# Optimization experiments

Measured on AMD Instinct MI355X. Metric: run time of the kernel, lower is better.

## Reference

```python
import jax, jax.numpy as jnp
import numpy as np
from jax import lax

B = 64          # graphs per batch
N0 = 1024       # nodes per graph (equal-sized graphs -> static topk shapes)
DEG = 16        # avg degree
E = B * N0 * DEG
D_IN, D_H, D_OUT = 100, 128, 256
RATIO, EPS = 0.5, 1e-5


def _seg_sum(v, idx, n):
    return jax.ops.segment_sum(v, idx, num_segments=n)


def _gcn(x, src, dst, w_e, W, b, n):
    h = x @ W
    deg = 1.0 + _seg_sum(w_e, dst, n)          # +1 for self-loop
    dinv = lax.rsqrt(deg)
    norm = (dinv[src] * dinv[dst] * w_e)[:, None]
    return _seg_sum(h[src] * norm, dst, n) + h / deg[:, None] + b


def _graphnorm(x, w, bias, ms, nb, k):
    # PyG GraphNorm: per-graph mean/var with learnable mean_scale
    xg = x.reshape(nb, k, -1)
    mean = xg.mean(1, keepdims=True)
    sub = xg - ms * mean
    var = (sub * sub).mean(1, keepdims=True)
    return (w * sub * lax.rsqrt(var + EPS) + bias).reshape(nb * k, -1)


def _topk(x, src, dst, emask, p, nb, n_per):
    # TopKPooling (min_score=None): score = tanh(x.p/||p||), keep top ceil(r*n)
    k = int(np.ceil(RATIO * n_per))
    score = jnp.tanh((x @ p) / jnp.linalg.norm(p))
    vals, idx = lax.top_k(score.reshape(nb, n_per), k)            # [nb, k]
    perm = (idx + (jnp.arange(nb) * n_per)[:, None]).reshape(-1)
    x_new = x[perm] * vals.reshape(-1)[:, None]
    mapping = jnp.full((nb * n_per,), -1, jnp.int32).at[perm].set(
        jnp.arange(nb * k, dtype=jnp.int32))
    ns, nd = mapping[src], mapping[dst]
    valid = emask & (ns >= 0) & (nd >= 0)   # filter_adj as a persistent mask
    return x_new, jnp.where(valid, ns, 0), jnp.where(valid, nd, 0), valid, k


def _forward(x, edge_index, W1, b1, W2, b2, W3, b3,
             gn1_w, gn1_b, gn1_ms, gn2_w, gn2_b, gn2_ms,
             gn3_w, gn3_b, gn3_ms, p1, p2, p3):
    src, dst = edge_index[0], edge_index[1]
    emask = jnp.ones(src.shape, bool)
    Ws, bs = (W1, W2, W3), (b1, b2, b3)
    gw = (gn1_w, gn2_w, gn3_w)
    gb = (gn1_b, gn2_b, gn3_b)
    gm = (gn1_ms, gn2_ms, gn3_ms)
    ps = (p1, p2, p3)
    n_per = N0
    for i in range(3):
        n = B * n_per
        x = _gcn(x, src, dst, emask.astype(x.dtype), Ws[i], bs[i], n)
        x = _graphnorm(x, gw[i], gb[i], gm[i], B, n_per)
        x = jax.nn.relu(x)              # dropout: identity in eval mode
        x, src, dst, emask, n_per = _topk(x, src, dst, emask, ps[i], B, n_per)
    xg = x.reshape(B, n_per, D_OUT)
    # global mean/max pool then concat -> [B, 2*D_OUT]
    return jnp.concatenate([xg.mean(1), xg.max(1)], axis=1)


def setup_inputs():
    key = jax.random.key(0)
    ks = jax.random.split(key, 20)
    x = jax.random.normal(ks[0], (B * N0, D_IN), jnp.float32)
    # random edges within each graph, then offset by graph base index
    e = jax.random.randint(ks[1], (2, B, N0 * DEG), 0, N0, jnp.int32)
    edge_index = (e + (jnp.arange(B, dtype=jnp.int32) * N0)[None, :, None]).reshape(2, -1)
    batch = jnp.repeat(jnp.arange(B, dtype=jnp.int32), N0)
    inp = dict(x=x, edge_index=edge_index, batch=batch)
    dims = [(D_IN, D_H), (D_H, D_H), (D_H, D_OUT)]
    for i, (di, do) in enumerate(dims, 1):
        inp[f"W{i}"] = jax.random.normal(ks[1 + i], (di, do), jnp.float32) / np.sqrt(di)
        inp[f"b{i}"] = jnp.zeros((do,), jnp.float32)
        inp[f"gn{i}_w"] = jnp.ones((do,), jnp.float32)
        inp[f"gn{i}_b"] = jnp.zeros((do,), jnp.float32)
        inp[f"gn{i}_ms"] = jnp.ones((do,), jnp.float32)
        inp[f"p{i}"] = jax.random.normal(ks[10 + i], (do,), jnp.float32)
    return inp


def reference(x, edge_index, batch, W1, b1, W2, b2, W3, b3,
              gn1_w, gn1_b, gn1_ms, gn2_w, gn2_b, gn2_ms,
              gn3_w, gn3_b, gn3_ms, p1, p2, p3):
    del batch  # equal-sized graphs: grouping is encoded by constants B, N0
    return _forward(x, edge_index, W1, b1, W2, b2, W3, b3,
                    gn1_w, gn1_b, gn1_ms, gn2_w, gn2_b, gn2_ms,
                    gn3_w, gn3_b, gn3_ms, p1, p2, p3)
```

## Files before the change

kernel.cpp:

```cpp
#include <hip/hip_runtime.h>

#define GN_EPS 1e-5f

constexpr int NB   = 64;
constexpr int EPG  = 16384;
constexpr int ETOT = NB * EPG;
constexpr int NTOT = 64 * 1024;

__global__ void cmap_init_kernel(int* __restrict__ cmap) {
    int i = blockIdx.x * blockDim.x + threadIdx.x;
    if (i < NTOT) cmap[i] = i;
}

template <int NPG>
__global__ __launch_bounds__(1024) void csr_build_kernel(
        const int* __restrict__ ei, int* __restrict__ cmap,
        const int* __restrict__ mapping, int do_compose,
        int* __restrict__ cnt, int* __restrict__ offs, float* __restrict__ dinv,
        int2* __restrict__ csr_pack) {
    __shared__ int   lcnt[NPG];
    __shared__ float sdv[NPG];
    __shared__ int   wsum[16];
    constexpr int NW = NPG / 64;
    const int g = blockIdx.x;
    const int t = threadIdx.x;
    const int ebase = g * EPG;
    constexpr int EPT = EPG / 1024;

    if (do_compose) {
        int i = g * 1024 + t;
        int c = cmap[i];
        cmap[i] = (c >= 0) ? mapping[c] : -1;
    }
    for (int i = t; i < NPG; i += 1024) lcnt[i] = 0;
    __syncthreads();

    int ms_[EPT], md_[EPT];
#pragma unroll
    for (int i = 0; i < EPT; i++) {
        int e = ebase + t + i * 1024;
        int s = cmap[ei[e]];
        int d = cmap[ei[ETOT + e]];
        bool ok = (s >= 0) && (d >= 0);
        ms_[i] = ok ? s : -1;
        md_[i] = ok ? (d - g * NPG) : 0;
        if (ok) atomicAdd(&lcnt[d - g * NPG], 1);
    }
    __syncthreads();

    const int lane = t & 63;
    const int wid  = t >> 6;
    int orig = (t < NPG) ? lcnt[t] : 0;
    int v = orig;
#pragma unroll
    for (int d = 1; d < 64; d <<= 1) {
        int u = __shfl_up(v, d);
        if (lane >= d) v += u;
    }
    if (lane == 63) wsum[wid] = v;
    __syncthreads();
    if (wid == 0) {
        int wv = (lane < NW) ? wsum[lane] : 0;
#pragma unroll
        for (int d = 1; d < 16; d <<= 1) {
            int u = __shfl_up(wv, d);
            if (lane >= d) wv += u;
        }
        if (lane < NW) wsum[lane] = wv;
    }
    __syncthreads();
    if (t < NPG) {
        int incl = v + ((wid > 0) ? wsum[wid - 1] : 0);
        int excl = incl - orig;
        float dv = rsqrtf(1.0f + (float)orig);
        cnt[g * NPG + t]  = orig;
        offs[g * NPG + t] = ebase + excl;
        dinv[g * NPG + t] = dv;
        sdv[t] = dv;
        lcnt[t] = excl;
    }
    __syncthreads();

#pragma unroll
    for (int i = 0; i < EPT; i++) {
        int s = ms_[i];
        if (s >= 0) {
            int pos = atomicAdd(&lcnt[md_[i]], 1);
            csr_pack[ebase + pos] = make_int2(s, __float_as_int(sdv[s - g * 1024 >= 0 && NPG == 1024 ? s - g * NPG : s - g * NPG]));
        }
    }
}

template <int D4>
__global__ __launch_bounds__(256) void gather_kernel(
        const float* __restrict__ x, const int* __restrict__ cnt,
        const int* __restrict__ offs, const float* __restrict__ dinv,
        const int2* __restrict__ csr_pack, float* __restrict__ z, int n, int bpg) {
    constexpr int GRP = 8;
    constexpr int NPB = 256 / GRP;
    constexpr int CPL = 4;
    int bid   = blockIdx.x;
    int xcd   = bid & 7;
    int slot  = bid >> 3;
    int graph = xcd + 8 * (slot / bpg);
    int local = slot % bpg;
    int vb    = graph * bpg + local;

    int grp  = threadIdx.x / GRP;
    int lane = threadIdx.x % GRP;
    int v = vb * NPB + grp;
    if (v >= n) return;

    const float4* x4 = reinterpret_cast<const float4*>(x);
    int st = offs[v];
    int c  = cnt[v];
    float dv = dinv[v];

    int f4_[CPL];
    bool act[CPL];
#pragma unroll
    for (int i = 0; i < CPL; i++) {
        f4_[i] = lane + GRP * i;
        act[i] = f4_[i] < D4;
    }

    float4 acc[CPL];
#pragma unroll
    for (int i = 0; i < CPL; i++) {
        if (act[i]) {
            float4 xv = x4[(size_t)v * D4 + f4_[i]];
            acc[i] = {xv.x * dv, xv.y * dv, xv.z * dv, xv.w * dv};
        } else {
            acc[i] = {0.f, 0.f, 0.f, 0.f};
        }
    }

    int j = 0;
    for (; j + 2 <= c; j += 2) {
        int2 p0 = csr_pack[st + j];
        int2 p1 = csr_pack[st + j + 1];
        float d0 = __int_as_float(p0.y);
        float d1 = __int_as_float(p1.y);
        size_t r0 = (size_t)p0.x * D4;
        size_t r1 = (size_t)p1.x * D4;
#pragma unroll
        for (int i = 0; i < CPL; i++) {
            if (!act[i]) continue;
            float4 h0 = x4[r0 + f4_[i]];
            float4 h1 = x4[r1 + f4_[i]];
            acc[i].x += h0.x * d0 + h1.x * d1;
            acc[i].y += h0.y * d0 + h1.y * d1;
            acc[i].z += h0.z * d0 + h1.z * d1;
            acc[i].w += h0.w * d0 + h1.w * d1;
        }
    }
    if (j < c) {
        int2 p0 = csr_pack[st + j];
        float d0 = __int_as_float(p0.y);
        size_t r0 = (size_t)p0.x * D4;
#pragma unroll
        for (int i = 0; i < CPL; i++) {
            if (!act[i]) continue;
            float4 h0 = x4[r0 + f4_[i]];
            acc[i].x += h0.x * d0; acc[i].y += h0.y * d0;
            acc[i].z += h0.z * d0; acc[i].w += h0.w * d0;
        }
    }
#pragma unroll
    for (int i = 0; i < CPL; i++) {
        if (!act[i]) continue;
        float4 o = {acc[i].x * dv, acc[i].y * dv, acc[i].z * dv, acc[i].w * dv};
        reinterpret_cast<float4*>(z)[(size_t)v * D4 + f4_[i]] = o;
    }
}

__global__ __launch_bounds__(256) void gemm128_kernel(const float* __restrict__ A,
                                                      const float* __restrict__ W,
                                                      const float* __restrict__ Bias,
                                                      float* __restrict__ C,
                                                      float* __restrict__ sum1,
                                                      float* __restrict__ sum2,
                                                      int M, int N, int K, int nper) {
    __shared__ float As[16][132];
    __shared__ float Bs[16][132];
    __shared__ float red1[4][132];
    __shared__ float red2[4][132];
    const int bm = blockIdx.x * 128;
    const int bn = blockIdx.y * 128;
    const int tid = threadIdx.x;
    const int tx = tid & 15, ty = tid >> 4;

    const int arow = tid >> 1;
    const int ak   = (tid & 1) * 8;
    const int brow = tid >> 5;
    const int bc4  = (tid & 31) * 4;

    float acc[2][2][4][4] = {};

    for (int k0 = 0; k0 < K; k0 += 16) {
        {
            const float* ap = A + (size_t)(bm + arow) * K + k0 + ak;
            float4 a0 = {0,0,0,0}, a1 = {0,0,0,0};
            if (k0 + ak < K)     a0 = *reinterpret_cast<const float4*>(ap);
            if (k0 + ak + 4 < K) a1 = *reinterpret_cast<const float4*>(ap + 4);
            As[ak + 0][arow] = a0.x; As[ak + 1][arow] = a0.y;
            As[ak + 2][arow] = a0.z; As[ak + 3][arow] = a0.w;
            As[ak + 4][arow] = a1.x; As[ak + 5][arow] = a1.y;
            As[ak + 6][arow] = a1.z; As[ak + 7][arow] = a1.w;
        }
        {
            float4 b0 = {0,0,0,0}, b1 = {0,0,0,0};
            if (k0 + brow < K)
                b0 = *reinterpret_cast<const float4*>(W + (size_t)(k0 + brow) * N + bn + bc4);
            if (k0 + brow + 8 < K)
                b1 = *reinterpret_cast<const float4*>(W + (size_t)(k0 + brow + 8) * N + bn + bc4);
            *reinterpret_cast<float4*>(&Bs[brow][bc4])     = b0;
            *reinterpret_cast<float4*>(&Bs[brow + 8][bc4]) = b1;
        }
        __syncthreads();
#pragma unroll
        for (int k = 0; k < 16; k++) {
            float4 a0 = *reinterpret_cast<const float4*>(&As[k][ty * 4]);
            float4 a1 = *reinterpret_cast<const float4*>(&As[k][64 + ty * 4]);
            float4 b0 = *reinterpret_cast<const float4*>(&Bs[k][tx * 4]);
            float4 b1 = *reinterpret_cast<const float4*>(&Bs[k][64 + tx * 4]);
            const float av[2][4] = {{a0.x, a0.y, a0.z, a0.w}, {a1.x, a1.y, a1.z, a1.w}};
            const float bv[2][4] = {{b0.x, b0.y, b0.z, b0.w}, {b1.x, b1.y, b1.z, b1.w}};
#pragma unroll
            for (int qi = 0; qi < 2; qi++)
#pragma unroll
                for (int qj = 0; qj < 2; qj++)
#pragma unroll
                    for (int i = 0; i < 4; i++)
#pragma unroll
                        for (int j = 0; j < 4; j++)
                            acc[qi][qj][i][j] += av[qi][i] * bv[qj][j];
        }
        __syncthreads();
    }
    float4 bb[2];
    bb[0] = *reinterpret_cast<const float4*>(&Bias[bn + tx * 4]);
    bb[1] = *reinterpret_cast<const float4*>(&Bias[bn + 64 + tx * 4]);

    float s1l[2][4] = {}, s2l[2][4] = {};
#pragma unroll
    for (int qi = 0; qi < 2; qi++)
#pragma unroll
        for (int i = 0; i < 4; i++) {
            int row = bm + qi * 64 + ty * 4 + i;
#pragma unroll
            for (int qj = 0; qj < 2; qj++) {
                float o0 = acc[qi][qj][i][0] + bb[qj].x;
                float o1 = acc[qi][qj][i][1] + bb[qj].y;
                float o2 = acc[qi][qj][i][2] + bb[qj].z;
                float o3 = acc[qi][qj][i][3] + bb[qj].w;
                float4 o = {o0, o1, o2, o3};
                *reinterpret_cast<float4*>(&C[(size_t)row * N + bn + qj * 64 + tx * 4]) = o;
                s1l[qj][0] += o0; s2l[qj][0] += o0 * o0;
                s1l[qj][1] += o1; s2l[qj][1] += o1 * o1;
                s1l[qj][2] += o2; s2l[qj][2] += o2 * o2;
                s1l[qj][3] += o3; s2l[qj][3] += o3 * o3;
            }
        }
    const int wv = tid >> 6;
#pragma unroll
    for (int qj = 0; qj < 2; qj++)
#pragma unroll
        for (int j = 0; j < 4; j++) {
            float v1 = s1l[qj][j], v2 = s2l[qj][j];
            v1 += __shfl_xor(v1, 16); v1 += __shfl_xor(v1, 32);
            v2 += __shfl_xor(v2, 16); v2 += __shfl_xor(v2, 32);
            if ((tid & 48) == 0) {
                red1[wv][tx * 8 + qj * 4 + j] = v1;
                red2[wv][tx * 8 + qj * 4 + j] = v2;
            }
        }
    __syncthreads();
    if (tid < 16) {
        const int g   = bm / nper;
        const int nch = nper >> 7;
        const int ch  = (bm % nper) >> 7;
        size_t slotbase = (size_t)(g * nch + ch) * N + bn;
#pragma unroll
        for (int qj = 0; qj < 2; qj++)
#pragma unroll
            for (int j = 0; j < 4; j++) {
                int k = tid * 8 + qj * 4 + j;
                float v1 = red1[0][k] + red1[1][k] + red1[2][k] + red1[3][k];
                float v2 = red2[0][k] + red2[1][k] + red2[2][k] + red2[3][k];
                sum1[slotbase + qj * 64 + tid * 4 + j] = v1;
                sum2[slotbase + qj * 64 + tid * 4 + j] = v2;
            }
    }
}

__global__ void pnorm3_kernel(const float* __restrict__ p0, const float* __restrict__ p1,
                              const float* __restrict__ p2, int d0, int d1, int d2,
                              float* __restrict__ out) {
    __shared__ float red[256];
    const float* p = (blockIdx.x == 0) ? p0 : (blockIdx.x == 1) ? p1 : p2;
    int d          = (blockIdx.x == 0) ? d0 : (blockIdx.x == 1) ? d1 : d2;
    int t = threadIdx.x;
    float v = (t < d) ? p[t] : 0.0f;
    red[t] = v * v;
    __syncthreads();
    for (int s = 128; s; s >>= 1) {
        if (t < s) red[t] += red[t + s];
        __syncthreads();
    }
    if (t == 0) out[blockIdx.x] = 1.0f / sqrtf(red[0]);
}

template <int DO>
__global__ __launch_bounds__(256) void gn_apply_score_kernel(
        float* __restrict__ x, const float* __restrict__ sum1, const float* __restrict__ sum2,
        const float* __restrict__ ms, const float* __restrict__ w,
        const float* __restrict__ bias, const float* __restrict__ p,
        const float* __restrict__ pinv, float* __restrict__ score, int n_per, int nch) {
    constexpr int V = DO / 64;
    __shared__ float scm[DO];
    __shared__ float ssr[DO];
    int node = blockIdx.x * 4 + (threadIdx.x >> 6);
    int lane = threadIdx.x & 63;
    int g = node / n_per;
    float inv_n = 1.0f / (float)n_per;
    for (int f = threadIdx.x; f < DO; f += 256) {
        float s1 = 0.f, s2 = 0.f;
        for (int ch = 0; ch < nch; ch++) {
            s1 += sum1[(size_t)(g * nch + ch) * DO + f];
            s2 += sum2[(size_t)(g * nch + ch) * DO + f];
        }
        float mean = s1 * inv_n;
        float ex2  = s2 * inv_n;
        float m = ms[f];
        float var = ex2 - 2.f * m * mean * mean + m * m * mean * mean;
        scm[f] = m * mean;
        ssr[f] = w[f] * rsqrtf(var + GN_EPS);
    }
    __syncthreads();

    float*       xr = x + (size_t)node * DO + lane * V;
    const float* bb = bias + lane * V;
    const float* pp = p + lane * V;
    float dot = 0.f;
#pragma unroll
    for (int i = 0; i < V; i++) {
        int f = lane * V + i;
        float y = (xr[i] - scm[f]) * ssr[f] + bb[i];
        y = fmaxf(y, 0.0f);
        xr[i] = y;
        dot += y * pp[i];
    }
#pragma unroll
    for (int off = 32; off; off >>= 1) dot += __shfl_xor(dot, off);
    if (lane == 0) score[node] = tanhf(dot * pinv[0]);
}

template <int N, int K>
__global__ __launch_bounds__(1024) void topk_radix_kernel(
        const float* __restrict__ score, int* __restrict__ mapping,
        int* __restrict__ inv) {
    __shared__ int hist[256];
    __shared__ int sscan[N];
    __shared__ int sbyte, sneed;
    const int g = blockIdx.x;
    const int t = threadIdx.x;
    float sc = score[g * N + t];
    unsigned u = __float_as_uint(sc);
    unsigned key = (u & 0x80000000u) ? ~u : (u | 0x80000000u);

    unsigned prefix = 0;
    int need = K;
#pragma unroll
    for (int shift = 24; shift >= 0; shift -= 8) {
        if (t < 256) hist[t] = 0;
        __syncthreads();
        unsigned hm = (shift == 24) ? 0u : (0xFFFFFFFFu << (shift + 8));
        if ((key & hm) == (prefix & hm))
            atomicAdd(&hist[(key >> shift) & 255], 1);
        __syncthreads();
        if (t < 256) sscan[t] = hist[t];
        __syncthreads();
        for (int d = 1; d < 256; d <<= 1) {
            int x = (t < 256 && t + d < 256) ? sscan[t + d] : 0;
            __syncthreads();
            if (t < 256) sscan[t] += x;
            __syncthreads();
        }
        if (t < 256) {
            int ge  = sscan[t];
            int gt_ = (t + 1 < 256) ? sscan[t + 1] : 0;
            if (ge >= need && gt_ < need) { sbyte = t; sneed = need - gt_; }
        }
        __syncthreads();
        prefix |= ((unsigned)sbyte << shift);
        need = sneed;
        __syncthreads();
    }
    bool gt = key > prefix;
    bool eq = (key == prefix);
    sscan[t] = (gt ? (1 << 16) : 0) | (eq ? 1 : 0);
    __syncthreads();
    for (int d = 1; d < N; d <<= 1) {
        int x = (t >= d) ? sscan[t - d] : 0;
        __syncthreads();
        sscan[t] += x;
        __syncthreads();
    }
    int incl   = sscan[t];
    int gtrank = (incl >> 16) - (gt ? 1 : 0);
    int eqrank = (incl & 0xFFFF) - (eq ? 1 : 0);
    int cntGT  = K - need;
    bool sel = gt || (eq && (eqrank < need));
    int old_g = g * N + t;
    if (sel) {
        int slot = gt ? gtrank : (cntGT + eqrank);
        mapping[old_g] = g * K + slot;
        inv[g * K + slot] = old_g;
    } else {
        mapping[old_g] = -1;
    }
}

__global__ void permute_scale_kernel(const float* __restrict__ x, const int* __restrict__ inv,
                                     const float* __restrict__ score, float* __restrict__ xn,
                                     int total, int ldof4) {
    int t = blockIdx.x * blockDim.x + threadIdx.x;
    if (t >= total) return;
    int node = t >> ldof4;
    int f4   = t & ((1 << ldof4) - 1);
    int dof4 = 1 << ldof4;
    int old = inv[node];
    float sc = score[old];
    float4 v = reinterpret_cast<const float4*>(x)[(size_t)old * dof4 + f4];
    float4 o = {v.x * sc, v.y * sc, v.z * sc, v.w * sc};
    reinterpret_cast<float4*>(xn)[t] = o;
}

__global__ __launch_bounds__(1024) void pool_sel_kernel(const float* __restrict__ x,
                                                        const int* __restrict__ inv,
                                                        const float* __restrict__ score,
                                                        float* __restrict__ out) {
    __shared__ float ssum[1024];
    __shared__ float smax[1024];
    int g = blockIdx.x;
    int f = threadIdx.x & 255;
    int ch = threadIdx.x >> 8;
    float s = 0.f, mx = -INFINITY;
    for (int i = ch; i < 128; i += 4) {
        int old = inv[g * 128 + i];
        float sc = score[old];
        float v = x[(size_t)old * 256 + f] * sc;
        s += v;
        mx = fmaxf(mx, v);
    }
    ssum[threadIdx.x] = s;
    smax[threadIdx.x] = mx;
    __syncthreads();
    if (ch == 0) {
#pragma unroll
        for (int c = 1; c < 4; c++) {
            s  += ssum[f + c * 256];
            mx  = fmaxf(mx, smax[f + c * 256]);
        }
        out[g * 512 + f]       = s / 128.0f;
        out[g * 512 + 256 + f] = mx;
    }
}

static inline int cdiv_h(int a, int b) { return (a + b - 1) / b; }

extern "C" void kernel_launch(void* const* d_in, const int* in_sizes, int n_in,
                              void* d_out, int out_size, void* d_ws, size_t ws_size,
                              hipStream_t stream) {
    (void)in_sizes; (void)n_in; (void)out_size; (void)ws_size;

    const float* x_in = (const float*)d_in[0];
    const int*   ei   = (const int*)d_in[1];
    const float* Wm[3]  = {(const float*)d_in[3],  (const float*)d_in[9],  (const float*)d_in[15]};
    const float* bv[3]  = {(const float*)d_in[4],  (const float*)d_in[10], (const float*)d_in[16]};
    const float* gnw[3] = {(const float*)d_in[5],  (const float*)d_in[11], (const float*)d_in[17]};
    const float* gnb[3] = {(const float*)d_in[6],  (const float*)d_in[12], (const float*)d_in[18]};
    const float* gnm[3] = {(const float*)d_in[7],  (const float*)d_in[13], (const float*)d_in[19]};
    const float* pv[3]  = {(const float*)d_in[8],  (const float*)d_in[14], (const float*)d_in[20]};

    size_t off = 0;
    auto alloc = [&](size_t bytes) {
        void* p = (char*)d_ws + off;
        off += (bytes + 255) & ~(size_t)255;
        return p;
    };
    float* X1      = (float*)alloc((size_t)65536 * 128 * 4);
    float* Z       = (float*)alloc((size_t)65536 * 128 * 4);
    float* X2      = (float*)alloc((size_t)32768 * 128 * 4);
    int2*  csr_pack= (int2*)alloc((size_t)ETOT * 8);
    int*   cmap    = (int*)alloc(NTOT * 4);
    int*   cnt     = (int*)alloc(65536 * 4);
    int*   offs    = (int*)alloc(65536 * 4);
    float* dinv    = (float*)alloc(65536 * 4);
    float* score   = (float*)alloc(65536 * 4);
    int*   mapping = (int*)alloc(65536 * 4);
    int*   inv     = (int*)alloc(32768 * 4);
    float* sum1    = (float*)alloc(64 * 8 * 256 * 4);
    float* sum2    = (float*)alloc(64 * 8 * 256 * 4);
    float* pinv    = (float*)alloc(256);

    const int nper[4] = {1024, 512, 256, 128};
    const int din[3]  = {100, 128, 128};
    const int dof[3]  = {128, 128, 256};

    cmap_init_kernel<<<NTOT / 256, 256, 0, stream>>>(cmap);
    pnorm3_kernel<<<3, 256, 0, stream>>>(pv[0], pv[1], pv[2], dof[0], dof[1], dof[2], pinv);

    for (int L = 0; L < 3; L++) {
        const int n    = NB * nper[L];
        const int k    = nper[L + 1];
        const int nn   = NB * k;
        const int D    = dof[L];
        const int dof4 = D / 4;
        const int ldof4 = (dof4 == 32) ? 5 : 6;
        const int nch  = nper[L] / 128;
        const float* xin = (L == 0) ? x_in : X2;

        if (nper[L] == 1024)
            csr_build_kernel<1024><<<NB, 1024, 0, stream>>>(ei, cmap, mapping, 0,
                                                            cnt, offs, dinv, csr_pack);
        else if (nper[L] == 512)
            csr_build_kernel<512><<<NB, 1024, 0, stream>>>(ei, cmap, mapping, 1,
                                                           cnt, offs, dinv, csr_pack);
        else
            csr_build_kernel<256><<<NB, 1024, 0, stream>>>(ei, cmap, mapping, 1,
                                                           cnt, offs, dinv, csr_pack);

        {
            const int NPB = 32;
            const int bpg = nper[L] / NPB;
            if (L == 0)
                gather_kernel<25><<<n / NPB, 256, 0, stream>>>(xin, cnt, offs, dinv,
                                                               csr_pack, Z, n, bpg);
            else
                gather_kernel<32><<<n / NPB, 256, 0, stream>>>(xin, cnt, offs, dinv,
                                                               csr_pack, Z, n, bpg);
        }

        gemm128_kernel<<<dim3(n / 128, D / 128), 256, 0, stream>>>(Z, Wm[L], bv[L], X1,
                                                                   sum1, sum2,
                                                                   n, D, din[L], nper[L]);

        if (D == 128)
            gn_apply_score_kernel<128><<<n / 4, 256, 0, stream>>>(X1, sum1, sum2, gnm[L],
                                                                  gnw[L], gnb[L], pv[L],
                                                                  pinv + L, score, nper[L], nch);
        else
            gn_apply_score_kernel<256><<<n / 4, 256, 0, stream>>>(X1, sum1, sum2, gnm[L],
                                                                  gnw[L], gnb[L], pv[L],
                                                                  pinv + L, score, nper[L], nch);

        if (nper[L] == 1024)
            topk_radix_kernel<1024, 512><<<NB, 1024, 0, stream>>>(score, mapping, inv);
        else if (nper[L] == 512)
            topk_radix_kernel<512, 256><<<NB, 512, 0, stream>>>(score, mapping, inv);
        else
            topk_radix_kernel<256, 128><<<NB, 256, 0, stream>>>(score, mapping, inv);

        if (L < 2) {
            int total = nn * dof4;
            permute_scale_kernel<<<cdiv_h(total, 256), 256, 0, stream>>>(
                X1, inv, score, X2, total, ldof4);
        } else {
            pool_sel_kernel<<<NB, 1024, 0, stream>>>(X1, inv, score, (float*)d_out);
        }
    }
}
```

Baseline: 320.1 us.

## Defer GraphNorm write-back into permute/pool kernels and use wave-shuffle scan in topk

The score kernel no longer writes the normalized, ReLU'd activations back to memory. It only computes scores, and the GraphNorm affine plus ReLU is recomputed inside the permute and pool kernels for the selected nodes only. This removes a full write of the activation tensor and re-applies normalization to only half the nodes, at the cost of recomputing the per-graph stats reduction in more blocks. The topk kernel's block-wide Hillis-Steele LDS scan is also replaced with a wave-level shuffle scan plus a small cross-wave pass, which cuts the number of barriers.

```diff
diff --git a/kernel.cpp b/kernel.cpp
--- a/kernel.cpp
+++ b/kernel.cpp
@@ -86,7 +86,7 @@
         int s = ms_[i];
         if (s >= 0) {
             int pos = atomicAdd(&lcnt[md_[i]], 1);
-            csr_pack[ebase + pos] = make_int2(s, __float_as_int(sdv[s - g * 1024 >= 0 && NPG == 1024 ? s - g * NPG : s - g * NPG]));
+            csr_pack[ebase + pos] = make_int2(s, __float_as_int(sdv[s - g * NPG]));
         }
     }
 }
@@ -312,34 +312,43 @@
 }
 
 template <int DO>
-__global__ __launch_bounds__(256) void gn_apply_score_kernel(
-        float* __restrict__ x, const float* __restrict__ sum1, const float* __restrict__ sum2,
+__device__ __forceinline__ void gn_stats_to_lds(
+        const float* __restrict__ sum1, const float* __restrict__ sum2,
         const float* __restrict__ ms, const float* __restrict__ w,
-        const float* __restrict__ bias, const float* __restrict__ p,
-        const float* __restrict__ pinv, float* __restrict__ score, int n_per, int nch) {
+        float* scm, float* ssr, int g, int n_per, int nch, int tid, int nthr) {
+    float inv_n = 1.0f / (float)n_per;
+    for (int f = tid; f < DO; f += nthr) {
+        float s1 = 0.f, s2 = 0.f;
+        for (int ch = 0; ch < nch; ch++) {
+            s1 += sum1[(size_t)(g * nch + ch) * DO + f];
+            s2 += sum2[(size_t)(g * nch + ch) * DO + f];
+        }
+        float mean = s1 * inv_n;
+        float ex2  = s2 * inv_n;
+        float m = ms[f];
+        float var = ex2 - 2.f * m * mean * mean + m * m * mean * mean;
+        scm[f] = m * mean;
+        ssr[f] = w[f] * rsqrtf(var + GN_EPS);
+    }
+}
+
+template <int DO>
+__global__ __launch_bounds__(256) void gn_score_kernel(
+        const float* __restrict__ x, const float* __restrict__ sum1,
+        const float* __restrict__ sum2, const float* __restrict__ ms,
+        const float* __restrict__ w, const float* __restrict__ bias,
+        const float* __restrict__ p, const float* __restrict__ pinv,
+        float* __restrict__ score, int n_per, int nch) {
     constexpr int V = DO / 64;
     __shared__ float scm[DO];
     __shared__ float ssr[DO];
     int node = blockIdx.x * 4 + (threadIdx.x >> 6);
     int lane = threadIdx.x & 63;
     int g = node / n_per;
-    float inv_n = 1.0f / (float)n_per;
-    for (int f = threadIdx.x; f < DO; f += 256) {
-        float s1 = 0.f, s2 = 0.f;
-        for (int ch = 0; ch < nch; ch++) {
-            s1 += sum1[(size_t)(g * nch + ch) * DO + f];
-            s2 += sum2[(size_t)(g * nch + ch) * DO + f];
-        }
-        float mean = s1 * inv_n;
-        float ex2  = s2 * inv_n;
-        float m = ms[f];
-        float var = ex2 - 2.f * m * mean * mean + m * m * mean * mean;
-        scm[f] = m * mean;
-        ssr[f] = w[f] * rsqrtf(var + GN_EPS);
-    }
-    __syncthreads();
-
-    float*       xr = x + (size_t)node * DO + lane * V;
+    gn_stats_to_lds<DO>(sum1, sum2, ms, w, scm, ssr, g, n_per, nch, threadIdx.x, 256);
+    __syncthreads();
+
+    const float* xr = x + (size_t)node * DO + lane * V;
     const float* bb = bias + lane * V;
     const float* pp = p + lane * V;
     float dot = 0.f;
@@ -348,7 +357,6 @@
         int f = lane * V + i;
         float y = (xr[i] - scm[f]) * ssr[f] + bb[i];
         y = fmaxf(y, 0.0f);
-        xr[i] = y;
         dot += y * pp[i];
     }
 #pragma unroll
@@ -361,8 +369,10 @@
         const float* __restrict__ score, int* __restrict__ mapping,
         int* __restrict__ inv) {
     __shared__ int hist[256];
-    __shared__ int sscan[N];
+    __shared__ int sscan[256];
+    __shared__ int wsum[16];
     __shared__ int sbyte, sneed;
+    constexpr int NW = N / 64;
     const int g = blockIdx.x;
     const int t = threadIdx.x;
     float sc = score[g * N + t];
@@ -399,15 +409,28 @@
     }
     bool gt = key > prefix;
     bool eq = (key == prefix);
-    sscan[t] = (gt ? (1 << 16) : 0) | (eq ? 1 : 0);
-    __syncthreads();
-    for (int d = 1; d < N; d <<= 1) {
-        int x = (t >= d) ? sscan[t - d] : 0;
-        __syncthreads();
-        sscan[t] += x;
-        __syncthreads();
-    }
-    int incl   = sscan[t];
+    int val = (gt ? (1 << 16) : 0) | (eq ? 1 : 0);
+    const int lane = t & 63;
+    const int wid  = t >> 6;
+    int v = val;
+#pragma unroll
+    for (int d = 1; d < 64; d <<= 1) {
+        int u2 = __shfl_up(v, d);
+        if (lane >= d) v += u2;
+    }
+    if (lane == 63) wsum[wid] = v;
+    __syncthreads();
+    if (wid == 0) {
+        int wv = (lane < NW) ? wsum[lane] : 0;
+#pragma unroll
+        for (int d = 1; d < 16; d <<= 1) {
+            int u2 = __shfl_up(wv, d);
+            if (lane >= d) wv += u2;
+        }
+        if (lane < NW) wsum[lane] = wv;
+    }
+    __syncthreads();
+    int incl = v + ((wid > 0) ? wsum[wid - 1] : 0);
     int gtrank = (incl >> 16) - (gt ? 1 : 0);
     int eqrank = (incl & 0xFFFF) - (eq ? 1 : 0);
     int cntGT  = K - need;
@@ -422,37 +445,60 @@
     }
 }
 
-__global__ void permute_scale_kernel(const float* __restrict__ x, const int* __restrict__ inv,
-                                     const float* __restrict__ score, float* __restrict__ xn,
-                                     int total, int ldof4) {
-    int t = blockIdx.x * blockDim.x + threadIdx.x;
-    if (t >= total) return;
-    int node = t >> ldof4;
-    int f4   = t & ((1 << ldof4) - 1);
-    int dof4 = 1 << ldof4;
+template <int DO>
+__global__ __launch_bounds__(256) void permute_norm_kernel(
+        const float* __restrict__ x, const int* __restrict__ inv,
+        const float* __restrict__ score, const float* __restrict__ sum1,
+        const float* __restrict__ sum2, const float* __restrict__ ms,
+        const float* __restrict__ w, const float* __restrict__ bias,
+        float* __restrict__ xn, int n_per, int nch, int kk) {
+    constexpr int V = DO / 64;
+    __shared__ float scm[DO];
+    __shared__ float ssr[DO];
+    int node = blockIdx.x * 4 + (threadIdx.x >> 6);
+    int lane = threadIdx.x & 63;
+    int g = node / kk;
+    gn_stats_to_lds<DO>(sum1, sum2, ms, w, scm, ssr, g, n_per, nch, threadIdx.x, 256);
+    __syncthreads();
+
     int old = inv[node];
     float sc = score[old];
-    float4 v = reinterpret_cast<const float4*>(x)[(size_t)old * dof4 + f4];
-    float4 o = {v.x * sc, v.y * sc, v.z * sc, v.w * sc};
-    reinterpret_cast<float4*>(xn)[t] = o;
-}
-
-__global__ __launch_bounds__(1024) void pool_sel_kernel(const float* __restrict__ x,
-                                                        const int* __restrict__ inv,
-                                                        const float* __restrict__ score,
-                                                        float* __restrict__ out) {
+    const float* xr = x + (size_t)old * DO + lane * V;
+    const float* bb = bias + lane * V;
+    float* xo = xn + (size_t)node * DO + lane * V;
+#pragma unroll
+    for (int i = 0; i < V; i++) {
+        int f = lane * V + i;
+        float y = (xr[i] - scm[f]) * ssr[f] + bb[i];
+        y = fmaxf(y, 0.0f);
+        xo[i] = y * sc;
+    }
+}
+
+__global__ __launch_bounds__(1024) void pool_sel_kernel(
+        const float* __restrict__ x, const int* __restrict__ inv,
+        const float* __restrict__ score, const float* __restrict__ sum1,
+        const float* __restrict__ sum2, const float* __restrict__ ms,
+        const float* __restrict__ w, const float* __restrict__ bias,
+        float* __restrict__ out, int n_per, int nch) {
+    __shared__ float scm[256];
+    __shared__ float ssr[256];
     __shared__ float ssum[1024];
     __shared__ float smax[1024];
     int g = blockIdx.x;
     int f = threadIdx.x & 255;
     int ch = threadIdx.x >> 8;
+    gn_stats_to_lds<256>(sum1, sum2, ms, w, scm, ssr, g, n_per, nch, threadIdx.x, 1024);
+    __syncthreads();
+    float cm = scm[f], sr = ssr[f], bb = bias[f];
     float s = 0.f, mx = -INFINITY;
     for (int i = ch; i < 128; i += 4) {
         int old = inv[g * 128 + i];
         float sc = score[old];
-        float v = x[(size_t)old * 256 + f] * sc;
-        s += v;
-        mx = fmaxf(mx, v);
+        float y = (x[(size_t)old * 256 + f] - cm) * sr + bb;
+        y = fmaxf(y, 0.0f) * sc;
+        s += y;
+        mx = fmaxf(mx, y);
     }
     ssum[threadIdx.x] = s;
     smax[threadIdx.x] = mx;
@@ -517,8 +563,6 @@
         const int k    = nper[L + 1];
         const int nn   = NB * k;
         const int D    = dof[L];
-        const int dof4 = D / 4;
-        const int ldof4 = (dof4 == 32) ? 5 : 6;
         const int nch  = nper[L] / 128;
         const float* xin = (L == 0) ? x_in : X2;
 
@@ -548,13 +592,13 @@
                                                                    n, D, din[L], nper[L]);
 
         if (D == 128)
-            gn_apply_score_kernel<128><<<n / 4, 256, 0, stream>>>(X1, sum1, sum2, gnm[L],
-                                                                  gnw[L], gnb[L], pv[L],
-                                                                  pinv + L, score, nper[L], nch);
+            gn_score_kernel<128><<<n / 4, 256, 0, stream>>>(X1, sum1, sum2, gnm[L], gnw[L],
+                                                            gnb[L], pv[L], pinv + L,
+                                                            score, nper[L], nch);
         else
-            gn_apply_score_kernel<256><<<n / 4, 256, 0, stream>>>(X1, sum1, sum2, gnm[L],
-                                                                  gnw[L], gnb[L], pv[L],
-                                                                  pinv + L, score, nper[L], nch);
+            gn_score_kernel<256><<<n / 4, 256, 0, stream>>>(X1, sum1, sum2, gnm[L], gnw[L],
+                                                            gnb[L], pv[L], pinv + L,
+                                                            score, nper[L], nch);
 
         if (nper[L] == 1024)
             topk_radix_kernel<1024, 512><<<NB, 1024, 0, stream>>>(score, mapping, inv);
@@ -564,11 +608,18 @@
             topk_radix_kernel<256, 128><<<NB, 256, 0, stream>>>(score, mapping, inv);
 
         if (L < 2) {
-            int total = nn * dof4;
-            permute_scale_kernel<<<cdiv_h(total, 256), 256, 0, stream>>>(
-                X1, inv, score, X2, total, ldof4);
+            if (D == 128)
+                permute_norm_kernel<128><<<nn / 4, 256, 0, stream>>>(
+                    X1, inv, score, sum1, sum2, gnm[L], gnw[L], gnb[L], X2,
+                    nper[L], nch, k);
+            else
+                permute_norm_kernel<256><<<nn / 4, 256, 0, stream>>>(
+                    X1, inv, score, sum1, sum2, gnm[L], gnw[L], gnb[L], X2,
+                    nper[L], nch, k);
         } else {
-            pool_sel_kernel<<<NB, 1024, 0, stream>>>(X1, inv, score, (float*)d_out);
-        }
-    }
-}
+            pool_sel_kernel<<<NB, 1024, 0, stream>>>(X1, inv, score, sum1, sum2,
+                                                     gnm[L], gnw[L], gnb[L],
+                                                     (float*)d_out, nper[L], nch);
+        }
+    }
+}
```

After: 329.4 us. 2.9% more time.
